# Kernel tuning notes

Measured on AMD Instinct MI355X. Metric: run time of the kernel, lower is better.

## Reference

```python
import jax, jax.numpy as jnp
import numpy as np

B, C_IN, C_OUT, N = 8, 256, 128, 4096
BN_EPS = 1e-5


def _conv1x1(w, b, t):
    # w: [out, in], t: [B, in, N] -> [B, out, N]
    return jnp.einsum('oc,bcn->bon', w, t) + b[None, :, None]


def setup_inputs() -> dict:
    key = jax.random.key(0)
    ks = jax.random.split(key, 11)
    s_in = 1.0 / np.sqrt(C_IN)
    s_out = 1.0 / np.sqrt(C_OUT)
    return {
        'x': jax.random.normal(ks[0], (B, C_IN, N), dtype=jnp.float32),
        'g_w': jax.random.normal(ks[1], (C_OUT, C_IN), dtype=jnp.float32) * s_in,
        'g_b': jax.random.normal(ks[2], (C_OUT,), dtype=jnp.float32) * s_in,
        'theta_w': jax.random.normal(ks[3], (C_OUT, C_IN), dtype=jnp.float32) * s_in,
        'theta_b': jax.random.normal(ks[4], (C_OUT,), dtype=jnp.float32) * s_in,
        'phi_w': jax.random.normal(ks[5], (C_OUT, C_IN), dtype=jnp.float32) * s_in,
        'phi_b': jax.random.normal(ks[6], (C_OUT,), dtype=jnp.float32) * s_in,
        'W_w': jax.random.normal(ks[7], (C_IN, C_OUT), dtype=jnp.float32) * s_out,
        'W_b': jax.random.normal(ks[8], (C_IN,), dtype=jnp.float32) * s_out,
        'bn_gamma': jax.random.uniform(ks[9], (C_IN,), dtype=jnp.float32),
        'bn_beta': jax.random.normal(ks[10], (C_IN,), dtype=jnp.float32) * 0.1,
    }


def reference(x, g_w, g_b, theta_w, theta_b, phi_w, phi_b, W_w, W_b, bn_gamma, bn_beta):
    n = x.shape[-1]
    g_x = _conv1x1(g_w, g_b, x)          # [B, Co, N]
    theta_x = _conv1x1(theta_w, theta_b, x)  # [B, Co, N]
    phi_x = _conv1x1(phi_w, phi_b, x)        # [B, Co, N]
    # f = theta_x^T @ phi_x, divided by N (no softmax) -> [B, N, N]
    f_div_c = jnp.einsum('bcn,bcm->bnm', theta_x, phi_x) / n
    # y[b,c,n] = sum_m f[b,n,m] * g_x[b,c,m]  -> already permuted to [B, Co, N]
    y = jnp.einsum('bnm,bcm->bcn', f_div_c, g_x)
    w_y = jnp.einsum('oc,bcn->bon', W_w, y) + W_b[None, :, None]  # [B, C_in, N]
    # BatchNorm1d, training mode: stats over (batch, spatial), biased variance
    mean = w_y.mean(axis=(0, 2), keepdims=True)
    var = w_y.var(axis=(0, 2), keepdims=True)
    w_y = (w_y - mean) * jax.lax.rsqrt(var + BN_EPS)
    w_y = w_y * bn_gamma[None, :, None] + bn_beta[None, :, None]
    return w_y + x  # generate=True residual
```

## Files before the change

### kernel.cpp

```cpp
#include <hip/hip_runtime.h>
#include <hip/hip_bf16.h>
#include <stdint.h>

#define BB   8
#define CIN  256
#define COUT 128
#define NN   4096

using f32x4  = __attribute__((ext_vector_type(4))) float;
using bf16x8 = __attribute__((ext_vector_type(8))) __bf16;
using u16x8  = __attribute__((ext_vector_type(8))) unsigned short;

static __device__ __forceinline__ unsigned short f2bf(float f) {
    unsigned int u = __builtin_bit_cast(unsigned int, f);
    u += 0x7FFFu + ((u >> 16) & 1u);
    return (unsigned short)(u >> 16);
}
static __device__ __forceinline__ bf16x8 pack8(float4 a, float4 b) {
    u16x8 r;
    r[0]=f2bf(a.x); r[1]=f2bf(a.y); r[2]=f2bf(a.z); r[3]=f2bf(a.w);
    r[4]=f2bf(b.x); r[5]=f2bf(b.y); r[6]=f2bf(b.z); r[7]=f2bf(b.w);
    return __builtin_bit_cast(bf16x8, r);
}
#define MFMA(a,b,c) __builtin_amdgcn_mfma_f32_16x16x32_bf16((a),(b),(c),0,0,0)

static __device__ __forceinline__ int sw64(int r, int c)  { return (r*64  + c) ^ ((r&7)<<3); }
static __device__ __forceinline__ int sw128(int r, int c) { return (r*128 + c) ^ ((r&7)<<3); }

__global__ __launch_bounds__(256) void k1_conv3(
    const float* __restrict__ x,
    const float* __restrict__ gw, const float* __restrict__ gb,
    const float* __restrict__ tw, const float* __restrict__ tb,
    const float* __restrict__ pw, const float* __restrict__ pb,
    unsigned short* __restrict__ G, unsigned short* __restrict__ T,
    unsigned short* __restrict__ P)
{
    __shared__ __align__(16) unsigned short As[128*64];
    __shared__ __align__(16) unsigned short Bs[128*64];
    int bid = blockIdx.x;
    int b   = bid / 96;
    int r96 = bid % 96;
    int tm  = r96 >> 5;
    int n0  = (r96 & 31) * 128;
    const float* W    = (tm==0) ? gw : (tm==1) ? tw : pw;
    const float* bias = (tm==0) ? gb : (tm==1) ? tb : pb;
    unsigned short* O = (tm==0) ? G  : (tm==1) ? T  : P;

    int t = threadIdx.x;
    int lane = t & 63, wv = t >> 6;
    int wr = wv >> 1, wc = wv & 1;
    int lr = lane & 15, lg = lane >> 4;

    f32x4 acc[4][4];
    #pragma unroll
    for (int i=0;i<4;i++)
        #pragma unroll
        for (int j=0;j<4;j++) acc[i][j] = (f32x4){0.f,0.f,0.f,0.f};

    const float* xb = x + (size_t)b * CIN * NN;

    for (int kc = 0; kc < 4; ++kc) {
        int k0 = kc * 64;
        {
            int rsub = t >> 4;
            int kq   = (t & 15) * 4;
            #pragma unroll
            for (int rr = 0; rr < 8; ++rr) {
                int row = rr*16 + rsub;
                float4 f = *(const float4*)(W + row*256 + k0 + kq);
                ushort4 pk; pk.x=f2bf(f.x); pk.y=f2bf(f.y); pk.z=f2bf(f.z); pk.w=f2bf(f.w);
                *(ushort4*)&As[sw64(row, kq)] = pk;
            }
        }
        {
            int nn_  = t & 127;
            int half = t >> 7;
            #pragma unroll
            for (int kk = 0; kk < 16; ++kk) {
                int p  = kk*2 + half;
                int kg = k0 + p*2;
                float f0 = xb[(size_t)kg*NN     + n0 + nn_];
                float f1 = xb[(size_t)(kg+1)*NN + n0 + nn_];
                unsigned int pk = (unsigned int)f2bf(f0) | ((unsigned int)f2bf(f1) << 16);
                *(unsigned int*)&Bs[sw64(nn_, p*2)] = pk;
            }
        }
        __syncthreads();
        #pragma unroll
        for (int kk = 0; kk < 2; ++kk) {
            bf16x8 af[4], bfr[4];
            #pragma unroll
            for (int mi=0; mi<4; ++mi) {
                int row = wr*64 + mi*16 + lr;
                af[mi] = __builtin_bit_cast(bf16x8, *(const u16x8*)&As[sw64(row, kk*32 + lg*8)]);
            }
            #pragma unroll
            for (int ni=0; ni<4; ++ni) {
                int row = wc*64 + ni*16 + lr;
                bfr[ni] = __builtin_bit_cast(bf16x8, *(const u16x8*)&Bs[sw64(row, kk*32 + lg*8)]);
            }
            #pragma unroll
            for (int mi=0; mi<4; ++mi)
                #pragma unroll
                for (int ni=0; ni<4; ++ni)
                    acc[mi][ni] = MFMA(af[mi], bfr[ni], acc[mi][ni]);
        }
        __syncthreads();
    }
    #pragma unroll
    for (int mi=0; mi<4; ++mi) {
        #pragma unroll
        for (int j=0; j<4; ++j) {
            int c = wr*64 + mi*16 + lg*4 + j;
            float bv = bias[c];
            #pragma unroll
            for (int ni=0; ni<4; ++ni) {
                int n = n0 + wc*64 + ni*16 + lr;
                O[(size_t)b*COUT*NN + (size_t)c*NN + n] = f2bf(acc[mi][ni][j] + bv);
            }
        }
    }
}

__global__ __launch_bounds__(256) void k2_m1(
    const unsigned short* __restrict__ P, const unsigned short* __restrict__ G,
    float* __restrict__ M1)
{
    __shared__ __align__(16) unsigned short Ps[128*64];
    __shared__ __align__(16) unsigned short Gs[128*64];
    int b  = blockIdx.x >> 4;
    int ks = blockIdx.x & 15;
    int t = threadIdx.x;
    int lane = t & 63, wv = t >> 6;
    int wr = wv >> 1, wc = wv & 1;
    int lr = lane & 15, lg = lane >> 4;

    f32x4 acc[4][4];
    #pragma unroll
    for (int i=0;i<4;i++)
        #pragma unroll
        for (int j=0;j<4;j++) acc[i][j] = (f32x4){0.f,0.f,0.f,0.f};

    const unsigned short* Pb = P + (size_t)b*COUT*NN;
    const unsigned short* Gb = G + (size_t)b*COUT*NN;

    for (int it = 0; it < 4; ++it) {
        int n0 = ks*256 + it*64;
        #pragma unroll
        for (int ss = 0; ss < 4; ++ss) {
            int idx = ss*256 + t;
            int row = idx >> 3;
            int c8  = (idx & 7) * 8;
            u16x8 v = *(const u16x8*)(Pb + (size_t)row*NN + n0 + c8);
            *(u16x8*)&Ps[sw64(row, c8)] = v;
            u16x8 g = *(const u16x8*)(Gb + (size_t)row*NN + n0 + c8);
            *(u16x8*)&Gs[sw64(row, c8)] = g;
        }
        __syncthreads();
        #pragma unroll
        for (int kk = 0; kk < 2; ++kk) {
            bf16x8 af[4], bfr[4];
            #pragma unroll
            for (int mi=0; mi<4; ++mi) {
                int row = wr*64 + mi*16 + lr;
                af[mi] = __builtin_bit_cast(bf16x8, *(const u16x8*)&Ps[sw64(row, kk*32 + lg*8)]);
            }
            #pragma unroll
            for (int ni=0; ni<4; ++ni) {
                int row = wc*64 + ni*16 + lr;
                bfr[ni] = __builtin_bit_cast(bf16x8, *(const u16x8*)&Gs[sw64(row, kk*32 + lg*8)]);
            }
            #pragma unroll
            for (int mi=0; mi<4; ++mi)
                #pragma unroll
                for (int ni=0; ni<4; ++ni)
                    acc[mi][ni] = MFMA(af[mi], bfr[ni], acc[mi][ni]);
        }
        __syncthreads();
    }
    float* m1b = M1 + (size_t)b*16384;
    #pragma unroll
    for (int mi=0; mi<4; ++mi)
        #pragma unroll
        for (int j=0; j<4; ++j) {
            int kch = wr*64 + mi*16 + lg*4 + j;
            #pragma unroll
            for (int ni=0; ni<4; ++ni) {
                int cch = wc*64 + ni*16 + lr;
                atomicAdd(&m1b[kch*128 + cch], acc[mi][ni][j]);
            }
        }
}

__global__ __launch_bounds__(256) void k3_w2(
    const float* __restrict__ Ww, const float* __restrict__ M1,
    unsigned short* __restrict__ W2)
{
    int b = blockIdx.x >> 2, q = blockIdx.x & 3;
    int wv = threadIdx.x >> 6, lane = threadIdx.x & 63;
    int lr = lane & 15, lg = lane >> 4;
    int o16 = q*64 + wv*16;

    bf16x8 a[4];
    const float* wrow = Ww + (size_t)(o16 + lr)*128;
    #pragma unroll
    for (int ksx=0; ksx<4; ++ksx) {
        float4 f0 = *(const float4*)(wrow + ksx*32 + lg*8);
        float4 f1 = *(const float4*)(wrow + ksx*32 + lg*8 + 4);
        a[ksx] = pack8(f0, f1);
    }
    const float* m1b = M1 + (size_t)b*16384;
    for (int kt = 0; kt < 8; ++kt) {
        f32x4 acc = (f32x4){0.f,0.f,0.f,0.f};
        const float* mrow = m1b + (size_t)(kt*16 + lr)*128;
        #pragma unroll
        for (int ksx=0; ksx<4; ++ksx) {
            float4 f0 = *(const float4*)(mrow + ksx*32 + lg*8);
            float4 f1 = *(const float4*)(mrow + ksx*32 + lg*8 + 4);
            bf16x8 bb = pack8(f0, f1);
            acc = MFMA(a[ksx], bb, acc);
        }
        #pragma unroll
        for (int j=0;j<4;++j) {
            int o = o16 + lg*4 + j;
            int k = kt*16 + lr;
            W2[(size_t)b*32768 + (size_t)o*128 + k] = f2bf(acc[j] * (1.0f/4096.0f));
        }
    }
}

__global__ __launch_bounds__(256) void k4_wy(
    const unsigned short* __restrict__ W2, const unsigned short* __restrict__ T,
    const float* __restrict__ Wb, float* __restrict__ out)
{
    __shared__ __align__(16) unsigned short As[128*128];
    __shared__ __align__(16) unsigned short Bs[128*128];
    int bid = blockIdx.x;
    int b   = bid >> 6;
    int r64 = bid & 63;
    int o0  = (r64 >> 5) * 128;
    int n0  = (r64 & 31) * 128;
    int t = threadIdx.x;
    int lane = t & 63, wv = t >> 6;
    int wr = wv >> 1, wc = wv & 1;
    int lr = lane & 15, lg = lane >> 4;

    #pragma unroll
    for (int ss = 0; ss < 8; ++ss) {
        int idx = ss*256 + t;
        int row = idx >> 4;
        int c8  = (idx & 15) * 8;
        u16x8 v = *(const u16x8*)(W2 + (size_t)b*32768 + (size_t)(o0+row)*128 + c8);
        *(u16x8*)&As[sw128(row, c8)] = v;
    }
    {
        int nn_  = t & 127;
        int half = t >> 7;
        const unsigned short* Tb = T + (size_t)b*COUT*NN + n0 + nn_;
        #pragma unroll
        for (int kk = 0; kk < 32; ++kk) {
            int p = kk*2 + half;
            unsigned int lo = Tb[(size_t)(2*p)*NN];
            unsigned int hi = Tb[(size_t)(2*p+1)*NN];
            *(unsigned int*)&Bs[sw128(nn_, p*2)] = lo | (hi << 16);
        }
    }
    __syncthreads();

    f32x4 acc[4][4];
    #pragma unroll
    for (int i=0;i<4;i++)
        #pragma unroll
        for (int j=0;j<4;j++) acc[i][j] = (f32x4){0.f,0.f,0.f,0.f};

    #pragma unroll
    for (int kk = 0; kk < 4; ++kk) {
        bf16x8 af[4], bfr[4];
        #pragma unroll
        for (int mi=0; mi<4; ++mi) {
            int row = wr*64 + mi*16 + lr;
            af[mi] = __builtin_bit_cast(bf16x8, *(const u16x8*)&As[sw128(row, kk*32 + lg*8)]);
        }
        #pragma unroll
        for (int ni=0; ni<4; ++ni) {
            int row = wc*64 + ni*16 + lr;
            bfr[ni] = __builtin_bit_cast(bf16x8, *(const u16x8*)&Bs[sw128(row, kk*32 + lg*8)]);
        }
        #pragma unroll
        for (int mi=0; mi<4; ++mi)
            #pragma unroll
            for (int ni=0; ni<4; ++ni)
                acc[mi][ni] = MFMA(af[mi], bfr[ni], acc[mi][ni]);
    }

    float* ob = out + (size_t)b*CIN*NN;
    #pragma unroll
    for (int mi=0; mi<4; ++mi)
        #pragma unroll
        for (int j=0; j<4; ++j) {
            int o = o0 + wr*64 + mi*16 + lg*4 + j;
            float bv = Wb[o];
            #pragma unroll
            for (int ni=0; ni<4; ++ni) {
                int n = n0 + wc*64 + ni*16 + lr;
                ob[(size_t)o*NN + n] = acc[mi][ni][j] + bv;
            }
        }
}

__global__ __launch_bounds__(256) void k5_stats(const float* __restrict__ wy,
                                                float* __restrict__ stats)
{
    int b = blockIdx.x >> 8, c = blockIdx.x & 255;
    const float4* p = (const float4*)(wy + (size_t)b*CIN*NN + (size_t)c*NN);
    float s1 = 0.f, s2 = 0.f;
    for (int i = threadIdx.x; i < 1024; i += 256) {
        float4 v = p[i];
        s1 += v.x + v.y + v.z + v.w;
        s2 += v.x*v.x + v.y*v.y + v.z*v.z + v.w*v.w;
    }
    for (int off = 32; off > 0; off >>= 1) {
        s1 += __shfl_down(s1, off);
        s2 += __shfl_down(s2, off);
    }
    __shared__ float r1[4], r2[4];
    int w = threadIdx.x >> 6;
    if ((threadIdx.x & 63) == 0) { r1[w] = s1; r2[w] = s2; }
    __syncthreads();
    if (threadIdx.x == 0) {
        s1 = r1[0]+r1[1]+r1[2]+r1[3];
        s2 = r2[0]+r2[1]+r2[2]+r2[3];
        atomicAdd(&stats[c], s1);
        atomicAdd(&stats[256 + c], s2);
    }
}

__global__ __launch_bounds__(256) void k6_final(
    float* __restrict__ out, const float* __restrict__ x,
    const float* __restrict__ stats, const float* __restrict__ gamma,
    const float* __restrict__ beta)
{
    const float inv = 1.0f / (float)(BB * NN);
    int stride = gridDim.x * blockDim.x;
    for (int i = blockIdx.x * blockDim.x + threadIdx.x; i < (BB*CIN*NN)/4; i += stride) {
        int c = (i >> 10) & 255;
        float mean = stats[c] * inv;
        float var  = stats[256 + c] * inv - mean*mean;
        float sc   = gamma[c] * rsqrtf(var + 1e-5f);
        float bb   = beta[c];
        float4 w  = ((const float4*)out)[i];
        float4 xv = ((const float4*)x)[i];
        float4 r;
        r.x = (w.x - mean)*sc + bb + xv.x;
        r.y = (w.y - mean)*sc + bb + xv.y;
        r.z = (w.z - mean)*sc + bb + xv.z;
        r.w = (w.w - mean)*sc + bb + xv.w;
        ((float4*)out)[i] = r;
    }
}

extern "C" void kernel_launch(void* const* d_in, const int* in_sizes, int n_in,
                              void* d_out, int out_size, void* d_ws, size_t ws_size,
                              hipStream_t stream)
{
    (void)in_sizes; (void)n_in; (void)out_size; (void)ws_size;
    const float* x     = (const float*)d_in[0];
    const float* gw    = (const float*)d_in[1];
    const float* gb    = (const float*)d_in[2];
    const float* tw    = (const float*)d_in[3];
    const float* tb    = (const float*)d_in[4];
    const float* pw    = (const float*)d_in[5];
    const float* pb    = (const float*)d_in[6];
    const float* Ww    = (const float*)d_in[7];
    const float* Wb    = (const float*)d_in[8];
    const float* gamma = (const float*)d_in[9];
    const float* beta  = (const float*)d_in[10];
    float* out = (float*)d_out;

    char* ws = (char*)d_ws;
    unsigned short* T  = (unsigned short*)(ws + 0);
    unsigned short* P  = (unsigned short*)(ws + 8388608);
    unsigned short* G  = (unsigned short*)(ws + 16777216);
    float* M1          = (float*)(ws + 25165824);
    float* stats       = (float*)(ws + 25690112);
    unsigned short* W2 = (unsigned short*)(ws + 25692160);

    hipMemsetAsync(ws + 25165824, 0, 524288 + 2048, stream);

    k1_conv3 <<<768,  256, 0, stream>>>(x, gw, gb, tw, tb, pw, pb, G, T, P);
    k2_m1    <<<128,  256, 0, stream>>>(P, G, M1);
    k3_w2    <<<32,   256, 0, stream>>>(Ww, M1, W2);
    k4_wy    <<<512,  256, 0, stream>>>(W2, T, Wb, out);
    k5_stats <<<2048, 256, 0, stream>>>(out, stats);
    k6_final <<<2048, 256, 0, stream>>>(out, x, stats, gamma, beta);
}
```

Baseline: 100.9 us.

## Restructure conv and W-projection kernels, fuse BN stats, store intermediates in bf16

Adds a prep kernel that converts and concatenates the three conv weights to bf16 and zeroes the accumulators, replacing the memset. The conv kernel now stages the whole x tile once in LDS and computes all three projections per block, writing theta transposed. The W projection kernel loads theta via direct global-to-LDS copies, writes w_y in bf16 and accumulates the BatchNorm sums in-block, which removes the separate stats kernel. The final kernel reads bf16 w_y, halving that traffic at some precision cost.

```diff
diff --git a/kernel.cpp b/kernel.cpp
--- a/kernel.cpp
+++ b/kernel.cpp
@@ -15,6 +15,12 @@
     unsigned int u = __builtin_bit_cast(unsigned int, f);
     u += 0x7FFFu + ((u >> 16) & 1u);
     return (unsigned short)(u >> 16);
+}
+static __device__ __forceinline__ float bf2f(unsigned short u) {
+    return __builtin_bit_cast(float, (unsigned int)u << 16);
+}
+static __device__ __forceinline__ ushort4 pack4(float a, float b, float c, float d) {
+    ushort4 r; r.x=f2bf(a); r.y=f2bf(b); r.z=f2bf(c); r.w=f2bf(d); return r;
 }
 static __device__ __forceinline__ bf16x8 pack8(float4 a, float4 b) {
     u16x8 r;
@@ -25,98 +31,126 @@
 #define MFMA(a,b,c) __builtin_amdgcn_mfma_f32_16x16x32_bf16((a),(b),(c),0,0,0)
 
 static __device__ __forceinline__ int sw64(int r, int c)  { return (r*64  + c) ^ ((r&7)<<3); }
-static __device__ __forceinline__ int sw128(int r, int c) { return (r*128 + c) ^ ((r&7)<<3); }
-
-__global__ __launch_bounds__(256) void k1_conv3(
-    const float* __restrict__ x,
-    const float* __restrict__ gw, const float* __restrict__ gb,
-    const float* __restrict__ tw, const float* __restrict__ tb,
-    const float* __restrict__ pw, const float* __restrict__ pb,
-    unsigned short* __restrict__ G, unsigned short* __restrict__ T,
-    unsigned short* __restrict__ P)
-{
-    __shared__ __align__(16) unsigned short As[128*64];
-    __shared__ __align__(16) unsigned short Bs[128*64];
-    int bid = blockIdx.x;
-    int b   = bid / 96;
-    int r96 = bid % 96;
-    int tm  = r96 >> 5;
-    int n0  = (r96 & 31) * 128;
-    const float* W    = (tm==0) ? gw : (tm==1) ? tw : pw;
-    const float* bias = (tm==0) ? gb : (tm==1) ? tb : pb;
-    unsigned short* O = (tm==0) ? G  : (tm==1) ? T  : P;
-
-    int t = threadIdx.x;
+
+typedef __attribute__((address_space(3))) unsigned int lds_uint;
+typedef __attribute__((address_space(1))) const unsigned int glob_uint;
+static __device__ __forceinline__ void glds16(const void* g, void* l) {
+    __builtin_amdgcn_global_load_lds((glob_uint*)g, (lds_uint*)l, 16, 0, 0);
+}
+
+__global__ __launch_bounds__(256) void z0_prep(
+    const float* __restrict__ gw, const float* __restrict__ pw, const float* __restrict__ tw,
+    const float* __restrict__ gb, const float* __restrict__ pb, const float* __restrict__ tb,
+    float* __restrict__ M1, float* __restrict__ stats,
+    unsigned short* __restrict__ Wcat, float* __restrict__ biascat)
+{
+    int t = blockIdx.x * 256 + threadIdx.x;
+    int gs = gridDim.x * 256;
+    float4 z = {0.f,0.f,0.f,0.f};
+    for (int i = t; i < 32768 + 128; i += gs) {
+        if (i < 32768) ((float4*)M1)[i] = z;
+        else ((float4*)stats)[i - 32768] = z;
+    }
+    for (int i = t; i < 24576; i += gs) {
+        int flat = i * 4;
+        int o = flat >> 8, c = flat & 255;
+        const float* src = (o < 128) ? (gw + o*256) : (o < 256) ? (pw + (o-128)*256) : (tw + (o-256)*256);
+        float4 f = *(const float4*)(src + c);
+        ushort4 u; u.x=f2bf(f.x); u.y=f2bf(f.y); u.z=f2bf(f.z); u.w=f2bf(f.w);
+        *(ushort4*)(Wcat + flat) = u;
+    }
+    if (t < 384)
+        biascat[t] = (t < 128) ? gb[t] : (t < 256) ? pb[t-128] : tb[t-256];
+}
+
+__global__ __launch_bounds__(512) void k1_conv3(
+    const float* __restrict__ x, const unsigned short* __restrict__ Wcat,
+    const float* __restrict__ biascat,
+    unsigned short* __restrict__ G, unsigned short* __restrict__ P,
+    unsigned short* __restrict__ TT)
+{
+    __shared__ __align__(16) unsigned short Xs[128*256];
+    int b  = blockIdx.x >> 5;
+    int n0 = (blockIdx.x & 31) * 128;
+    int t  = threadIdx.x;
+
+    {
+        int c  = t & 255;
+        int nq = (t >> 8) * 64;
+        const float* xp = x + ((size_t)b*CIN + c)*NN + n0 + nq;
+        #pragma unroll
+        for (int r = 0; r < 16; ++r) {
+            float4 f = *(const float4*)(xp + r*4);
+            int n = nq + r*4;
+            Xs[(n+0)*256 + (c ^ (((n+0)&7)<<3))] = f2bf(f.x);
+            Xs[(n+1)*256 + (c ^ (((n+1)&7)<<3))] = f2bf(f.y);
+            Xs[(n+2)*256 + (c ^ (((n+2)&7)<<3))] = f2bf(f.z);
+            Xs[(n+3)*256 + (c ^ (((n+3)&7)<<3))] = f2bf(f.w);
+        }
+    }
+    __syncthreads();
+
     int lane = t & 63, wv = t >> 6;
-    int wr = wv >> 1, wc = wv & 1;
+    int wr = wv >> 2, wc = wv & 3;
     int lr = lane & 15, lg = lane >> 4;
-
-    f32x4 acc[4][4];
+    int nb = wr*64, ob = wc*96;
+
+    f32x4 acc[4][6];
     #pragma unroll
     for (int i=0;i<4;i++)
         #pragma unroll
-        for (int j=0;j<4;j++) acc[i][j] = (f32x4){0.f,0.f,0.f,0.f};
-
-    const float* xb = x + (size_t)b * CIN * NN;
-
-    for (int kc = 0; kc < 4; ++kc) {
-        int k0 = kc * 64;
-        {
-            int rsub = t >> 4;
-            int kq   = (t & 15) * 4;
-            #pragma unroll
-            for (int rr = 0; rr < 8; ++rr) {
-                int row = rr*16 + rsub;
-                float4 f = *(const float4*)(W + row*256 + k0 + kq);
-                ushort4 pk; pk.x=f2bf(f.x); pk.y=f2bf(f.y); pk.z=f2bf(f.z); pk.w=f2bf(f.w);
-                *(ushort4*)&As[sw64(row, kq)] = pk;
+        for (int j=0;j<6;j++) acc[i][j] = (f32x4){0.f,0.f,0.f,0.f};
+
+    #pragma unroll
+    for (int ks = 0; ks < 8; ++ks) {
+        bf16x8 xf[4], wf[6];
+        #pragma unroll
+        for (int ni = 0; ni < 4; ++ni) {
+            int n = nb + ni*16 + lr;
+            int cq = (ks*4 + lg) ^ (n & 7);
+            xf[ni] = __builtin_bit_cast(bf16x8, *(const u16x8*)&Xs[n*256 + cq*8]);
+        }
+        #pragma unroll
+        for (int os = 0; os < 6; ++os) {
+            int o = ob + os*16 + lr;
+            wf[os] = __builtin_bit_cast(bf16x8, *(const u16x8*)(Wcat + (size_t)o*256 + ks*32 + lg*8));
+        }
+        #pragma unroll
+        for (int os = 0; os < 6; ++os) {
+            bool th = (ob + os*16) >= 256;
+            #pragma unroll
+            for (int ni = 0; ni < 4; ++ni)
+                acc[ni][os] = th ? MFMA(wf[os], xf[ni], acc[ni][os])
+                                 : MFMA(xf[ni], wf[os], acc[ni][os]);
+        }
+    }
+
+    unsigned short* Gb  = G  + (size_t)b*COUT*NN;
+    unsigned short* Pb  = P  + (size_t)b*COUT*NN;
+    unsigned short* TTb = TT + (size_t)b*NN*COUT;
+    #pragma unroll
+    for (int os = 0; os < 6; ++os) {
+        int o = ob + os*16;
+        if (o < 256) {
+            float bv = biascat[o + lr];
+            unsigned short* dst = ((o < 128) ? (Gb + (size_t)(o + lr)*NN)
+                                             : (Pb + (size_t)(o - 128 + lr)*NN)) + n0 + nb;
+            #pragma unroll
+            for (int ni = 0; ni < 4; ++ni) {
+                f32x4 v = acc[ni][os];
+                *(ushort4*)(dst + ni*16 + lg*4) = pack4(v[0]+bv, v[1]+bv, v[2]+bv, v[3]+bv);
             }
-        }
-        {
-            int nn_  = t & 127;
-            int half = t >> 7;
-            #pragma unroll
-            for (int kk = 0; kk < 16; ++kk) {
-                int p  = kk*2 + half;
-                int kg = k0 + p*2;
-                float f0 = xb[(size_t)kg*NN     + n0 + nn_];
-                float f1 = xb[(size_t)(kg+1)*NN + n0 + nn_];
-                unsigned int pk = (unsigned int)f2bf(f0) | ((unsigned int)f2bf(f1) << 16);
-                *(unsigned int*)&Bs[sw64(nn_, p*2)] = pk;
-            }
-        }
-        __syncthreads();
-        #pragma unroll
-        for (int kk = 0; kk < 2; ++kk) {
-            bf16x8 af[4], bfr[4];
-            #pragma unroll
-            for (int mi=0; mi<4; ++mi) {
-                int row = wr*64 + mi*16 + lr;
-                af[mi] = __builtin_bit_cast(bf16x8, *(const u16x8*)&As[sw64(row, kk*32 + lg*8)]);
-            }
-            #pragma unroll
-            for (int ni=0; ni<4; ++ni) {
-                int row = wc*64 + ni*16 + lr;
-                bfr[ni] = __builtin_bit_cast(bf16x8, *(const u16x8*)&Bs[sw64(row, kk*32 + lg*8)]);
-            }
-            #pragma unroll
-            for (int mi=0; mi<4; ++mi)
-                #pragma unroll
-                for (int ni=0; ni<4; ++ni)
-                    acc[mi][ni] = MFMA(af[mi], bfr[ni], acc[mi][ni]);
-        }
-        __syncthreads();
-    }
-    #pragma unroll
-    for (int mi=0; mi<4; ++mi) {
-        #pragma unroll
-        for (int j=0; j<4; ++j) {
-            int c = wr*64 + mi*16 + lg*4 + j;
-            float bv = bias[c];
-            #pragma unroll
-            for (int ni=0; ni<4; ++ni) {
-                int n = n0 + wc*64 + ni*16 + lr;
-                O[(size_t)b*COUT*NN + (size_t)c*NN + n] = f2bf(acc[mi][ni][j] + bv);
+        } else {
+            int c0 = o - 256 + lg*4;
+            float b0 = biascat[o + lg*4 + 0];
+            float b1 = biascat[o + lg*4 + 1];
+            float b2 = biascat[o + lg*4 + 2];
+            float b3 = biascat[o + lg*4 + 3];
+            #pragma unroll
+            for (int ni = 0; ni < 4; ++ni) {
+                int n = n0 + nb + ni*16 + lr;
+                f32x4 v = acc[ni][os];
+                *(ushort4*)(TTb + (size_t)n*COUT + c0) = pack4(v[0]+b0, v[1]+b1, v[2]+b2, v[3]+b3);
             }
         }
     }
@@ -229,133 +263,114 @@
     }
 }
 
-__global__ __launch_bounds__(256) void k4_wy(
-    const unsigned short* __restrict__ W2, const unsigned short* __restrict__ T,
-    const float* __restrict__ Wb, float* __restrict__ out)
-{
-    __shared__ __align__(16) unsigned short As[128*128];
-    __shared__ __align__(16) unsigned short Bs[128*128];
-    int bid = blockIdx.x;
-    int b   = bid >> 6;
-    int r64 = bid & 63;
-    int o0  = (r64 >> 5) * 128;
-    int n0  = (r64 & 31) * 128;
-    int t = threadIdx.x;
+__global__ __launch_bounds__(512) void k4_wy(
+    const unsigned short* __restrict__ W2, const unsigned short* __restrict__ TT,
+    const float* __restrict__ Wb, unsigned short* __restrict__ WY,
+    float* __restrict__ stats)
+{
+    __shared__ __align__(16) unsigned short Ts[128*128];
+    __shared__ float sb[512];
+    int b  = blockIdx.x >> 5;
+    int n0 = (blockIdx.x & 31) * 128;
+    int t  = threadIdx.x;
     int lane = t & 63, wv = t >> 6;
-    int wr = wv >> 1, wc = wv & 1;
+    sb[t] = 0.f;
+
+    const unsigned short* TTb = TT + ((size_t)b*NN + n0)*COUT;
+    #pragma unroll
+    for (int g = 0; g < 4; ++g) {
+        int nl = wv*16 + g*4 + (lane >> 4);
+        int kq = lane & 15;
+        const unsigned short* src = TTb + (size_t)nl*128 + ((kq ^ (nl & 7)) * 8);
+        glds16(src, &Ts[(wv*16 + g*4) * 128]);
+    }
+    asm volatile("s_waitcnt vmcnt(0)");
+    __syncthreads();
+
+    int wr = wv >> 2, wo = wv & 3;
     int lr = lane & 15, lg = lane >> 4;
-
-    #pragma unroll
-    for (int ss = 0; ss < 8; ++ss) {
-        int idx = ss*256 + t;
-        int row = idx >> 4;
-        int c8  = (idx & 15) * 8;
-        u16x8 v = *(const u16x8*)(W2 + (size_t)b*32768 + (size_t)(o0+row)*128 + c8);
-        *(u16x8*)&As[sw128(row, c8)] = v;
-    }
-    {
-        int nn_  = t & 127;
-        int half = t >> 7;
-        const unsigned short* Tb = T + (size_t)b*COUT*NN + n0 + nn_;
-        #pragma unroll
-        for (int kk = 0; kk < 32; ++kk) {
-            int p = kk*2 + half;
-            unsigned int lo = Tb[(size_t)(2*p)*NN];
-            unsigned int hi = Tb[(size_t)(2*p+1)*NN];
-            *(unsigned int*)&Bs[sw128(nn_, p*2)] = lo | (hi << 16);
+    int nb = wr*64, ob = wo*64;
+    const unsigned short* W2b = W2 + (size_t)b*32768;
+
+    f32x4 acc[4][4];
+    #pragma unroll
+    for (int i=0;i<4;i++)
+        #pragma unroll
+        for (int j=0;j<4;j++) acc[i][j] = (f32x4){0.f,0.f,0.f,0.f};
+
+    #pragma unroll
+    for (int ks = 0; ks < 4; ++ks) {
+        bf16x8 tf[4], wf[4];
+        #pragma unroll
+        for (int ni = 0; ni < 4; ++ni) {
+            int n = nb + ni*16 + lr;
+            int kq = (ks*4 + lg) ^ (n & 7);
+            tf[ni] = __builtin_bit_cast(bf16x8, *(const u16x8*)&Ts[n*128 + kq*8]);
+        }
+        #pragma unroll
+        for (int oi = 0; oi < 4; ++oi) {
+            int o = ob + oi*16 + lr;
+            wf[oi] = __builtin_bit_cast(bf16x8, *(const u16x8*)(W2b + (size_t)o*128 + ks*32 + lg*8));
+        }
+        #pragma unroll
+        for (int ni = 0; ni < 4; ++ni)
+            #pragma unroll
+            for (int oi = 0; oi < 4; ++oi)
+                acc[ni][oi] = MFMA(tf[ni], wf[oi], acc[ni][oi]);
+    }
+
+    unsigned short* wyb = WY + (size_t)b*CIN*NN;
+    #pragma unroll
+    for (int oi = 0; oi < 4; ++oi) {
+        int o = ob + oi*16 + lr;
+        float bv = Wb[o];
+        float s1 = 0.f, s2 = 0.f;
+        #pragma unroll
+        for (int ni = 0; ni < 4; ++ni) {
+            f32x4 v = acc[ni][oi];
+            float v0 = v[0]+bv, v1 = v[1]+bv, v2 = v[2]+bv, v3 = v[3]+bv;
+            s1 += v0+v1+v2+v3;
+            s2 += v0*v0+v1*v1+v2*v2+v3*v3;
+            *(ushort4*)(wyb + (size_t)o*NN + n0 + nb + ni*16 + lg*4) = pack4(v0,v1,v2,v3);
+        }
+        s1 += __shfl_xor(s1, 16); s1 += __shfl_xor(s1, 32);
+        s2 += __shfl_xor(s2, 16); s2 += __shfl_xor(s2, 32);
+        if (lg == 0) {
+            atomicAdd(&sb[o], s1);
+            atomicAdd(&sb[256 + o], s2);
         }
     }
     __syncthreads();
-
-    f32x4 acc[4][4];
-    #pragma unroll
-    for (int i=0;i<4;i++)
-        #pragma unroll
-        for (int j=0;j<4;j++) acc[i][j] = (f32x4){0.f,0.f,0.f,0.f};
-
-    #pragma unroll
-    for (int kk = 0; kk < 4; ++kk) {
-        bf16x8 af[4], bfr[4];
-        #pragma unroll
-        for (int mi=0; mi<4; ++mi) {
-            int row = wr*64 + mi*16 + lr;
-            af[mi] = __builtin_bit_cast(bf16x8, *(const u16x8*)&As[sw128(row, kk*32 + lg*8)]);
-        }
-        #pragma unroll
-        for (int ni=0; ni<4; ++ni) {
-            int row = wc*64 + ni*16 + lr;
-            bfr[ni] = __builtin_bit_cast(bf16x8, *(const u16x8*)&Bs[sw128(row, kk*32 + lg*8)]);
-        }
-        #pragma unroll
-        for (int mi=0; mi<4; ++mi)
-            #pragma unroll
-            for (int ni=0; ni<4; ++ni)
-                acc[mi][ni] = MFMA(af[mi], bfr[ni], acc[mi][ni]);
-    }
-
-    float* ob = out + (size_t)b*CIN*NN;
-    #pragma unroll
-    for (int mi=0; mi<4; ++mi)
-        #pragma unroll
-        for (int j=0; j<4; ++j) {
-            int o = o0 + wr*64 + mi*16 + lg*4 + j;
-            float bv = Wb[o];
-            #pragma unroll
-            for (int ni=0; ni<4; ++ni) {
-                int n = n0 + wc*64 + ni*16 + lr;
-                ob[(size_t)o*NN + n] = acc[mi][ni][j] + bv;
-            }
-        }
-}
-
-__global__ __launch_bounds__(256) void k5_stats(const float* __restrict__ wy,
-                                                float* __restrict__ stats)
-{
-    int b = blockIdx.x >> 8, c = blockIdx.x & 255;
-    const float4* p = (const float4*)(wy + (size_t)b*CIN*NN + (size_t)c*NN);
-    float s1 = 0.f, s2 = 0.f;
-    for (int i = threadIdx.x; i < 1024; i += 256) {
-        float4 v = p[i];
-        s1 += v.x + v.y + v.z + v.w;
-        s2 += v.x*v.x + v.y*v.y + v.z*v.z + v.w*v.w;
-    }
-    for (int off = 32; off > 0; off >>= 1) {
-        s1 += __shfl_down(s1, off);
-        s2 += __shfl_down(s2, off);
-    }
-    __shared__ float r1[4], r2[4];
-    int w = threadIdx.x >> 6;
-    if ((threadIdx.x & 63) == 0) { r1[w] = s1; r2[w] = s2; }
-    __syncthreads();
-    if (threadIdx.x == 0) {
-        s1 = r1[0]+r1[1]+r1[2]+r1[3];
-        s2 = r2[0]+r2[1]+r2[2]+r2[3];
-        atomicAdd(&stats[c], s1);
-        atomicAdd(&stats[256 + c], s2);
-    }
+    atomicAdd(&stats[t], sb[t]);
 }
 
 __global__ __launch_bounds__(256) void k6_final(
-    float* __restrict__ out, const float* __restrict__ x,
+    const unsigned short* __restrict__ WY, const float* __restrict__ x,
     const float* __restrict__ stats, const float* __restrict__ gamma,
-    const float* __restrict__ beta)
+    const float* __restrict__ beta, float* __restrict__ out)
 {
     const float inv = 1.0f / (float)(BB * NN);
     int stride = gridDim.x * blockDim.x;
-    for (int i = blockIdx.x * blockDim.x + threadIdx.x; i < (BB*CIN*NN)/4; i += stride) {
-        int c = (i >> 10) & 255;
+    for (int i = blockIdx.x * blockDim.x + threadIdx.x; i < (BB*CIN*NN)/8; i += stride) {
+        int c = (i >> 9) & 255;
         float mean = stats[c] * inv;
         float var  = stats[256 + c] * inv - mean*mean;
         float sc   = gamma[c] * rsqrtf(var + 1e-5f);
         float bb   = beta[c];
-        float4 w  = ((const float4*)out)[i];
-        float4 xv = ((const float4*)x)[i];
-        float4 r;
-        r.x = (w.x - mean)*sc + bb + xv.x;
-        r.y = (w.y - mean)*sc + bb + xv.y;
-        r.z = (w.z - mean)*sc + bb + xv.z;
-        r.w = (w.w - mean)*sc + bb + xv.w;
-        ((float4*)out)[i] = r;
+        u16x8 w = ((const u16x8*)WY)[i];
+        float4 x0 = ((const float4*)x)[i*2];
+        float4 x1 = ((const float4*)x)[i*2+1];
+        float4 r0, r1;
+        r0.x = (bf2f(w[0]) - mean)*sc + bb + x0.x;
+        r0.y = (bf2f(w[1]) - mean)*sc + bb + x0.y;
+        r0.z = (bf2f(w[2]) - mean)*sc + bb + x0.z;
+        r0.w = (bf2f(w[3]) - mean)*sc + bb + x0.w;
+        r1.x = (bf2f(w[4]) - mean)*sc + bb + x1.x;
+        r1.y = (bf2f(w[5]) - mean)*sc + bb + x1.y;
+        r1.z = (bf2f(w[6]) - mean)*sc + bb + x1.z;
+        r1.w = (bf2f(w[7]) - mean)*sc + bb + x1.w;
+        ((float4*)out)[i*2]   = r0;
+        ((float4*)out)[i*2+1] = r1;
     }
 }
 
@@ -378,19 +393,20 @@
     float* out = (float*)d_out;
 
     char* ws = (char*)d_ws;
-    unsigned short* T  = (unsigned short*)(ws + 0);
-    unsigned short* P  = (unsigned short*)(ws + 8388608);
-    unsigned short* G  = (unsigned short*)(ws + 16777216);
-    float* M1          = (float*)(ws + 25165824);
-    float* stats       = (float*)(ws + 25690112);
-    unsigned short* W2 = (unsigned short*)(ws + 25692160);
-
-    hipMemsetAsync(ws + 25165824, 0, 524288 + 2048, stream);
-
-    k1_conv3 <<<768,  256, 0, stream>>>(x, gw, gb, tw, tb, pw, pb, G, T, P);
-    k2_m1    <<<128,  256, 0, stream>>>(P, G, M1);
-    k3_w2    <<<32,   256, 0, stream>>>(Ww, M1, W2);
-    k4_wy    <<<512,  256, 0, stream>>>(W2, T, Wb, out);
-    k5_stats <<<2048, 256, 0, stream>>>(out, stats);
-    k6_final <<<2048, 256, 0, stream>>>(out, x, stats, gamma, beta);
-}
+    unsigned short* G    = (unsigned short*)(ws + 0);
+    unsigned short* P    = (unsigned short*)(ws + (8u<<20));
+    unsigned short* WY   = (unsigned short*)(ws + 0);
+    unsigned short* TT   = (unsigned short*)(ws + (16u<<20));
+    float* M1            = (float*)(ws + (24u<<20));
+    unsigned short* W2   = (unsigned short*)(ws + (24u<<20) + 524288);
+    unsigned short* Wcat = (unsigned short*)(ws + (25u<<20));
+    float* biascat       = (float*)(ws + (25u<<20) + 196608);
+    float* stats         = (float*)(ws + (25u<<20) + 198656);
+
+    z0_prep <<<128,  256, 0, stream>>>(gw, pw, tw, gb, pb, tb, M1, stats, Wcat, biascat);
+    k1_conv3<<<256,  512, 0, stream>>>(x, Wcat, biascat, G, P, TT);
+    k2_m1   <<<128,  256, 0, stream>>>(P, G, M1);
+    k3_w2   <<<32,   256, 0, stream>>>(Ww, M1, W2);
+    k4_wy   <<<256,  512, 0, stream>>>(W2, TT, Wb, WY, stats);
+    k6_final<<<2048, 256, 0, stream>>>(WY, x, stats, gamma, beta, out);
+}
```

Result: faster. 98.90 us (-2.0%).
